# Kernel optimization log

Hardware: AMD Instinct MI355X
Metric: run time of the kernel (lower is better)

The kernel has to match this reference:

```python
import math
import jax, jax.numpy as jnp
import numpy as np

B, T, H, A, F = 2, 2048, 2048, 2048, 8192
L, LID, EPS = 24, 0, 1e-5
NEG_INF = -1e38


def setup_inputs() -> dict:
    key = jax.random.key(0)
    ks = jax.random.split(key, 8)
    s = 0.02
    # RWKV init-derived time parameters for layer_id=0, num_hidden_layers=24
    ratio_0_to_1 = LID / (L - 1)          # 0.0
    ratio_1_to_almost_0 = 1.0 - LID / L    # 1.0
    x = jnp.arange(H, dtype=jnp.float32) / H
    tmk = jnp.power(x, ratio_1_to_almost_0)
    tmv = tmk + 0.3 * ratio_0_to_1
    tmr = jnp.power(x, 0.5 * ratio_1_to_almost_0)
    zigzag = 0.5 * (jnp.arange(1, A + 1, dtype=jnp.float32) % 3 - 1)
    time_first = jnp.full((A,), math.log(0.3), dtype=jnp.float32) + zigzag
    h = jnp.arange(A, dtype=jnp.float32)
    time_decay = -5.0 + 8.0 * (h / (A - 1)) ** (0.7 + 1.3 * ratio_0_to_1)
    return {
        'hidden': jax.random.normal(ks[0], (B, T, H), jnp.float32),
        'pre_w': jnp.ones((H,), jnp.float32), 'pre_b': jnp.zeros((H,), jnp.float32),
        'ln1_w': jnp.ones((H,), jnp.float32), 'ln1_b': jnp.zeros((H,), jnp.float32),
        'ln2_w': jnp.ones((H,), jnp.float32), 'ln2_b': jnp.zeros((H,), jnp.float32),
        'time_decay': time_decay, 'time_first': time_first,
        'tmk': tmk, 'tmv': tmv, 'tmr': tmr,
        'Wk': jax.random.normal(ks[1], (H, A), jnp.float32) * s,
        'Wv': jax.random.normal(ks[2], (H, A), jnp.float32) * s,
        'Wr': jax.random.normal(ks[3], (H, A), jnp.float32) * s,
        'Wo': jax.random.normal(ks[4], (A, H), jnp.float32) * s,
        'f_tmk': jnp.power(x, ratio_1_to_almost_0), 'f_tmr': jnp.power(x, ratio_1_to_almost_0),
        'f_Wk': jax.random.normal(ks[5], (H, F), jnp.float32) * s,
        'f_Wr': jax.random.normal(ks[6], (H, H), jnp.float32) * s,
        'f_Wv': jax.random.normal(ks[7], (F, H), jnp.float32) * s,
    }


def _ln(x, w, b):
    mu = x.mean(-1, keepdims=True)
    var = ((x - mu) ** 2).mean(-1, keepdims=True)
    return (x - mu) * jax.lax.rsqrt(var + EPS) * w + b


def _token_shift(x):
    # sx state is zeros at init: prepend a zero row, drop the last token
    return jnp.concatenate((jnp.zeros_like(x[:, :1, :]), x[:, :-1, :]), axis=1)


def _forward(hidden, pre_w, pre_b, ln1_w, ln1_b, ln2_w, ln2_b,
             time_decay, time_first, tmk, tmv, tmr, Wk, Wv, Wr, Wo,
             f_tmk, f_tmr, f_Wk, f_Wr, f_Wv):
    h0 = _ln(hidden, pre_w, pre_b)          # pre_ln (layer_id == 0)
    # ---- time mixing (RwkvSelfAttention) ----
    x1 = _ln(h0, ln1_w, ln1_b)
    cx = _token_shift(x1)
    kx = x1 * tmk + cx * (1 - tmk)
    vx = x1 * tmv + cx * (1 - tmv)
    rx = x1 * tmr + cx * (1 - tmr)
    r = jax.nn.sigmoid(rx @ Wr)             # [B,T,A]
    k = kx @ Wk
    v = vx @ Wv
    w_decay = -jnp.exp(time_decay)          # [A]

    def step(carry, kv):
        aa, bb, pp = carry                  # each [B,A]
        kk, vv = kv                         # each [B,A]
        ww = time_first + kk
        q = jnp.maximum(pp, ww)
        e1 = jnp.exp(pp - q)
        e2 = jnp.exp(ww - q)
        out = (e1 * aa + e2 * vv) / (e1 * bb + e2)
        ww2 = w_decay + pp
        q2 = jnp.maximum(ww2, kk)
        e1 = jnp.exp(ww2 - q2)
        e2 = jnp.exp(kk - q2)
        return (e1 * aa + e2 * vv, e1 * bb + e2, q2), out

    init = (jnp.zeros((B, A), k.dtype), jnp.zeros((B, A), k.dtype),
            jnp.full((B, A), NEG_INF, jnp.float32))
    _, wkv = jax.lax.scan(step, init, (jnp.swapaxes(k, 0, 1), jnp.swapaxes(v, 0, 1)))
    wkv = jnp.swapaxes(wkv, 0, 1)           # [B,T,A]
    h1 = h0 + (r * wkv) @ Wo
    # ---- channel mixing (RwkvFeedForward) ----
    x2 = _ln(h1, ln2_w, ln2_b)
    cx2 = _token_shift(x2)
    kx2 = x2 * f_tmk + cx2 * (1 - f_tmk)
    rx2 = x2 * f_tmr + cx2 * (1 - f_tmr)
    r2 = jax.nn.sigmoid(rx2 @ f_Wr)
    kk2 = jnp.square(jax.nn.relu(kx2 @ f_Wk))
    return h1 + r2 * (kk2 @ f_Wv)


def reference(hidden, pre_w, pre_b, ln1_w, ln1_b, ln2_w, ln2_b,
              time_decay, time_first, tmk, tmv, tmr, Wk, Wv, Wr, Wo,
              f_tmk, f_tmr, f_Wk, f_Wr, f_Wv):
    return _forward(hidden, pre_w, pre_b, ln1_w, ln1_b, ln2_w, ln2_b,
                    time_decay, time_first, tmk, tmv, tmr, Wk, Wv, Wr, Wo,
                    f_tmk, f_tmr, f_Wk, f_Wr, f_Wv)
```

## Files before the change

kernel.cpp:

```cpp
#include <hip/hip_runtime.h>

#define B_  2
#define T_  2048
#define H_  2048
#define A_  2048
#define F_  8192
#define BT_ 4096

typedef __bf16  bf16x8 __attribute__((ext_vector_type(8)));
typedef float   f32x4  __attribute__((ext_vector_type(4)));
typedef short   short8 __attribute__((ext_vector_type(8)));

__device__ __forceinline__ float bf2f(unsigned short b) {
  return __uint_as_float(((unsigned)b) << 16);
}
__device__ __forceinline__ unsigned short f2bf(float f) {
  unsigned u = __float_as_uint(f);
  unsigned r = (u + 0x7FFFu + ((u >> 16) & 1u)) >> 16;
  return (unsigned short)r;
}

typedef __attribute__((address_space(3))) void lds_void_t;
typedef __attribute__((address_space(1))) const void gc_void_t;
__device__ __forceinline__ void gload_lds16(const void* g, void* l) {
  __builtin_amdgcn_global_load_lds((gc_void_t*)g, (lds_void_t*)l, 16, 0, 0);
}

__global__ void canary_kernel(float* out) { out[threadIdx.x] = 1000.0f; }

__global__ __launch_bounds__(256) void transpose_bf16_kernel(
    const float* __restrict__ src, unsigned short* __restrict__ dst, int Kd, int Nd)
{
  __shared__ float tile[32][33];
  const int tx = threadIdx.x & 31;
  const int ty = threadIdx.x >> 5;
  const int n0 = blockIdx.x * 32;
  const int k0 = blockIdx.y * 32;
#pragma unroll
  for (int i = 0; i < 32; i += 8)
    tile[ty + i][tx] = src[(size_t)(k0 + ty + i) * Nd + n0 + tx];
  __syncthreads();
#pragma unroll
  for (int i = 0; i < 32; i += 8)
    dst[(size_t)(n0 + ty + i) * Kd + k0 + tx] = f2bf(tile[tx][ty + i]);
}

__device__ __forceinline__ void block_reduce2(float& a, float& b) {
#pragma unroll
  for (int off = 32; off > 0; off >>= 1) {
    a += __shfl_down(a, off, 64);
    b += __shfl_down(b, off, 64);
  }
  __shared__ float sa[4], sb[4];
  const int lane = threadIdx.x & 63, w = threadIdx.x >> 6;
  __syncthreads();
  if (lane == 0) { sa[w] = a; sb[w] = b; }
  __syncthreads();
  a = sa[0] + sa[1] + sa[2] + sa[3];
  b = sb[0] + sb[1] + sb[2] + sb[3];
}

__global__ __launch_bounds__(256) void ln_pre_kernel(
    const float* __restrict__ hidden,
    const float* __restrict__ pw, const float* __restrict__ pb,
    const float* __restrict__ w1, const float* __restrict__ b1,
    float* __restrict__ h0, unsigned short* __restrict__ x1)
{
  const int row = blockIdx.x, tid = threadIdx.x;
  const int c0 = tid * 8;
  const size_t base = (size_t)row * H_ + c0;
  float x[8];
  float4 v0 = *(const float4*)(hidden + base);
  float4 v1 = *(const float4*)(hidden + base + 4);
  x[0]=v0.x; x[1]=v0.y; x[2]=v0.z; x[3]=v0.w;
  x[4]=v1.x; x[5]=v1.y; x[6]=v1.z; x[7]=v1.w;
  float s = 0.f, s2 = 0.f;
#pragma unroll
  for (int j = 0; j < 8; ++j) { s += x[j]; s2 += x[j]*x[j]; }
  block_reduce2(s, s2);
  float mu  = s * (1.f / H_);
  float inv = rsqrtf(fmaxf(s2 * (1.f / H_) - mu*mu, 0.f) + 1e-5f);
  float y[8];
#pragma unroll
  for (int j = 0; j < 8; ++j) y[j] = (x[j] - mu) * inv * pw[c0+j] + pb[c0+j];
  *(float4*)(h0 + base)     = make_float4(y[0],y[1],y[2],y[3]);
  *(float4*)(h0 + base + 4) = make_float4(y[4],y[5],y[6],y[7]);
  s = 0.f; s2 = 0.f;
#pragma unroll
  for (int j = 0; j < 8; ++j) { s += y[j]; s2 += y[j]*y[j]; }
  block_reduce2(s, s2);
  mu  = s * (1.f / H_);
  inv = rsqrtf(fmaxf(s2 * (1.f / H_) - mu*mu, 0.f) + 1e-5f);
  unsigned o[4];
#pragma unroll
  for (int p = 0; p < 4; ++p) {
    unsigned lo = f2bf((y[2*p]   - mu) * inv * w1[c0+2*p]   + b1[c0+2*p]);
    unsigned hi = f2bf((y[2*p+1] - mu) * inv * w1[c0+2*p+1] + b1[c0+2*p+1]);
    o[p] = lo | (hi << 16);
  }
  *(uint4*)(x1 + base) = make_uint4(o[0], o[1], o[2], o[3]);
}

__global__ __launch_bounds__(256) void lnmix2_kernel(
    const float* __restrict__ h1,
    const float* __restrict__ w_, const float* __restrict__ b_,
    const float* __restrict__ tmk_, const float* __restrict__ tmr_,
    unsigned short* __restrict__ kx2b, unsigned short* __restrict__ rx2b)
{
  const int row = blockIdx.x, tid = threadIdx.x;
  const int t = row & (T_ - 1);
  const int c0 = tid * 8;
  const size_t base = (size_t)row * H_ + c0;
  float x[8], p[8];
  {
    float4 v0 = *(const float4*)(h1 + base);
    float4 v1 = *(const float4*)(h1 + base + 4);
    x[0]=v0.x; x[1]=v0.y; x[2]=v0.z; x[3]=v0.w;
    x[4]=v1.x; x[5]=v1.y; x[6]=v1.z; x[7]=v1.w;
  }
  const bool hasp = (t > 0);
  if (hasp) {
    float4 v0 = *(const float4*)(h1 + base - H_);
    float4 v1 = *(const float4*)(h1 + base - H_ + 4);
    p[0]=v0.x; p[1]=v0.y; p[2]=v0.z; p[3]=v0.w;
    p[4]=v1.x; p[5]=v1.y; p[6]=v1.z; p[7]=v1.w;
  } else {
#pragma unroll
    for (int j = 0; j < 8; ++j) p[j] = 0.f;
  }
  float s = 0.f, s2 = 0.f;
#pragma unroll
  for (int j = 0; j < 8; ++j) { s += x[j]; s2 += x[j]*x[j]; }
  block_reduce2(s, s2);
  const float mu  = s * (1.f / H_);
  const float inv = rsqrtf(fmaxf(s2 * (1.f / H_) - mu*mu, 0.f) + 1e-5f);
  float sp = 0.f, sp2 = 0.f;
#pragma unroll
  for (int j = 0; j < 8; ++j) { sp += p[j]; sp2 += p[j]*p[j]; }
  block_reduce2(sp, sp2);
  const float mup  = sp * (1.f / H_);
  const float invp = rsqrtf(fmaxf(sp2 * (1.f / H_) - mup*mup, 0.f) + 1e-5f);
  unsigned ok[4], orr[4];
#pragma unroll
  for (int q = 0; q < 4; ++q) {
    unsigned ko = 0, ro = 0;
#pragma unroll
    for (int h = 0; h < 2; ++h) {
      const int j = q*2 + h;
      const float xr = (x[j] - mu) * inv * w_[c0+j] + b_[c0+j];
      const float cr = hasp ? (p[j] - mup) * invp * w_[c0+j] + b_[c0+j] : 0.f;
      ko |= (unsigned)f2bf(fmaf(xr - cr, tmk_[c0+j], cr)) << (h*16);
      ro |= (unsigned)f2bf(fmaf(xr - cr, tmr_[c0+j], cr)) << (h*16);
    }
    ok[q] = ko; orr[q] = ro;
  }
  *(uint4*)(kx2b + base) = make_uint4(ok[0],ok[1],ok[2],ok[3]);
  *(uint4*)(rx2b + base) = make_uint4(orr[0],orr[1],orr[2],orr[3]);
}

__global__ __launch_bounds__(256) void mix1_kernel(
    const unsigned short* __restrict__ x,
    const float* __restrict__ tm_,
    unsigned short* __restrict__ outb)
{
  const int row = blockIdx.x;
  const int t = row & (T_ - 1);
  const int c0 = threadIdx.x * 8;
  const size_t base = (size_t)row * H_ + c0;
  uint4 xv = *(const uint4*)(x + base);
  uint4 cv = make_uint4(0u,0u,0u,0u);
  if (t > 0) cv = *(const uint4*)(x + base - H_);
  const unsigned xs[4] = {xv.x, xv.y, xv.z, xv.w};
  const unsigned cs[4] = {cv.x, cv.y, cv.z, cv.w};
  unsigned oo[4];
#pragma unroll
  for (int p = 0; p < 4; ++p) {
    unsigned w = 0;
#pragma unroll
    for (int h = 0; h < 2; ++h) {
      const int j = p*2 + h;
      float xf = bf2f((unsigned short)((xs[p] >> (h*16)) & 0xFFFFu));
      float cf = bf2f((unsigned short)((cs[p] >> (h*16)) & 0xFFFFu));
      w |= (unsigned)f2bf(fmaf(xf - cf, tm_[c0+j], cf)) << (h*16);
    }
    oo[p] = w;
  }
  *(uint4*)(outb + base) = make_uint4(oo[0],oo[1],oo[2],oo[3]);
}

#define WKV_G 32
#define WKV_C 32
#define WKV_L 64

__global__ __launch_bounds__(1024) void wkv_scan_kernel(
    const unsigned short* __restrict__ kg, const unsigned short* __restrict__ vg,
    const unsigned short* __restrict__ rg,
    const float* __restrict__ time_first, const float* __restrict__ time_decay,
    unsigned short* __restrict__ rwkv)
{
  const int tid = threadIdx.x;
  const int al  = tid & (WKV_G - 1);
  const int c   = tid >> 5;
  const int b   = blockIdx.x >> 6;
  const int ag  = blockIdx.x & 63;
  const int a   = ag * WKV_G + al;
  const float tf = time_first[a];
  const float w  = -__expf(time_decay[a]);
  const size_t cb = (size_t)b * T_ * A_ + a + (size_t)c * WKV_L * A_;

  float aa = 0.f, bb = 0.f, pp = -1e38f;
  {
    float kb[4], vb[4];
#pragma unroll
    for (int j = 0; j < 4; ++j) {
      kb[j] = bf2f(kg[cb + (size_t)j * A_]);
      vb[j] = bf2f(vg[cb + (size_t)j * A_]);
    }
    for (int t0 = 0; t0 < WKV_L; t0 += 4) {
#pragma unroll
      for (int j = 0; j < 4; ++j) {
        const float kk = kb[j], vv = vb[j];
        const int tn = t0 + j + 4;
        if (tn < WKV_L) {
          kb[j] = bf2f(kg[cb + (size_t)tn * A_]);
          vb[j] = bf2f(vg[cb + (size_t)tn * A_]);
        }
        float ww2 = w + pp;
        float q2  = fmaxf(ww2, kk);
        float e1  = __expf(ww2 - q2);
        float e2  = __expf(kk  - q2);
        aa = e1*aa + e2*vv;
        bb = e1*bb + e2;
        pp = q2;
      }
    }
  }
  __shared__ float saa[WKV_C][WKV_G], sbb[WKV_C][WKV_G], spp[WKV_C][WKV_G];
  saa[c][al] = aa; sbb[c][al] = bb; spp[c][al] = pp;
  __syncthreads();

  if (tid < WKV_G) {
    float Aa = 0.f, Bb = 0.f, Pp = -1e38f;
    const float Lw = (float)WKV_L * w;
    for (int cc = 0; cc < WKV_C; ++cc) {
      const float na = saa[cc][tid], nb = sbb[cc][tid], np = spp[cc][tid];
      saa[cc][tid] = Aa; sbb[cc][tid] = Bb; spp[cc][tid] = Pp;
      const float p1 = Pp + Lw;
      const float pc = fmaxf(p1, np);
      const float f1 = __expf(p1 - pc);
      const float f2 = __expf(np - pc);
      Aa = f1*Aa + f2*na;
      Bb = f1*Bb + f2*nb;
      Pp = pc;
    }
  }
  __syncthreads();
  aa = saa[c][al]; bb = sbb[c][al]; pp = spp[c][al];

  {
    float kb[4], vb[4], rb[4];
#pragma unroll
    for (int j = 0; j < 4; ++j) {
      kb[j] = bf2f(kg[cb + (size_t)j * A_]);
      vb[j] = bf2f(vg[cb + (size_t)j * A_]);
      rb[j] = bf2f(rg[cb + (size_t)j * A_]);
    }
    for (int t0 = 0; t0 < WKV_L; t0 += 4) {
#pragma unroll
      for (int j = 0; j < 4; ++j) {
        const float kk = kb[j], vv = vb[j], rr = rb[j];
        const int tn = t0 + j + 4;
        if (tn < WKV_L) {
          kb[j] = bf2f(kg[cb + (size_t)tn * A_]);
          vb[j] = bf2f(vg[cb + (size_t)tn * A_]);
          rb[j] = bf2f(rg[cb + (size_t)tn * A_]);
        }
        float ww = tf + kk;
        float q  = fmaxf(pp, ww);
        float e1 = __expf(pp - q);
        float e2 = __expf(ww - q);
        float o  = (e1*aa + e2*vv) / (e1*bb + e2);
        float sr = 1.f / (1.f + __expf(-rr));
        rwkv[cb + (size_t)(t0 + j) * A_] = f2bf(sr * o);
        float ww2 = w + pp;
        float q2  = fmaxf(ww2, kk);
        e1 = __expf(ww2 - q2);
        e2 = __expf(kk  - q2);
        aa = e1*aa + e2*vv;
        bb = e1*bb + e2;
        pp = q2;
      }
    }
  }
}

enum { EPI_BF16 = 0, EPI_ADDIP = 1, EPI_RELU2 = 2, EPI_SIGADD = 3 };

template <int BM, int NBUF, int RG, int CG, int EPI>
__global__ __launch_bounds__(512) void gemm4_kernel(
    const unsigned short* __restrict__ Ap, const unsigned short* __restrict__ Bp,
    void* __restrict__ Cp, int K, int Nn,
    const unsigned short* __restrict__ sigb)
{
  constexpr int BN = 256;
  constexpr int FM = BM / 32;
  constexpr int FN = 4;
  __shared__ unsigned short As[NBUF * BM * 64];
  __shared__ unsigned short Bs[NBUF * BN * 64];
  const int tid  = threadIdx.x;
  const int lane = tid & 63;
  const int lr = lane & 15;
  const int hi = lane >> 4;
  const int rx7 = lr & 7;
  const int wid = tid >> 6;
  const int wm = wid >> 2, wn = wid & 3;
  const int rowW = wm * (BM / 2);
  const int colW = wn * 64;
  const int gx = gridDim.x;
  const int gy = gridDim.y;
  const int flat = blockIdx.y * gx + blockIdx.x;
  const int xcd = flat & 7;
  const int j = flat >> 3;
  const int rgc = gy / RG;
  const int r_idx = xcd % rgc;
  const int c_idx = xcd / rgc;
  const int row_l = j % RG;
  const int col_l = j / RG;
  const long row0 = (long)(r_idx * RG + row_l) * BM;
  const long col0 = (long)(c_idx * CG + col_l) * BN;
  const unsigned short* Ab = Ap + (size_t)row0 * K;
  const unsigned short* Bb = Bp + (size_t)col0 * K;
  const int srow8 = tid >> 3;
  const int sslot = (tid & 7) ^ (srow8 & 7);
  f32x4 acc[FM][FN] = {};

  auto SP0 = [&](int bufi, int tt) {
    unsigned short* asb = As + bufi * (BM * 64);
    unsigned short* bsb = Bs + bufi * (BN * 64);
    const size_t ko = (size_t)tt * 64 + sslot * 8;
    gload_lds16(Ab + (size_t)srow8        * K + ko, asb + tid * 8);
    gload_lds16(Ab + (size_t)(srow8 + 64) * K + ko, asb + 4096 + tid * 8);
    gload_lds16(Bb + (size_t)srow8        * K + ko, bsb + tid * 8);
  };
  auto SP1 = [&](int bufi, int tt) {
    unsigned short* bsb = Bs + bufi * (BN * 64);
    const size_t ko = (size_t)tt * 64 + sslot * 8;
    gload_lds16(Bb + (size_t)(srow8 + 64)  * K + ko, bsb + 4096  + tid * 8);
    gload_lds16(Bb + (size_t)(srow8 + 128) * K + ko, bsb + 8192  + tid * 8);
    gload_lds16(Bb + (size_t)(srow8 + 192) * K + ko, bsb + 12288 + tid * 8);
  };
  auto SPq = [&](int bufi, int tt, int q) {
    const size_t ko = (size_t)tt * 64 + sslot * 8;
    if (q < 2) {
      unsigned short* asb = As + bufi * (BM * 64);
      gload_lds16(Ab + (size_t)(srow8 + q*128)      * K + ko, asb + q*8192 + tid * 8);
      gload_lds16(Ab + (size_t)(srow8 + q*128 + 64) * K + ko, asb + q*8192 + 4096 + tid * 8);
    } else {
      const int qq = q - 2;
      unsigned short* bsb = Bs + bufi * (BN * 64);
      gload_lds16(Bb + (size_t)(srow8 + qq*128)      * K + ko, bsb + qq*8192 + tid * 8);
      gload_lds16(Bb + (size_t)(srow8 + qq*128 + 64) * K + ko, bsb + qq*8192 + 4096 + tid * 8);
    }
  };

  const int nt = K >> 6;
  if constexpr (BM == 128) {
    SP0(0, 0); SP1(0, 0);
    if constexpr (NBUF == 3) { SP0(1, 1); SP1(1, 1); }
  } else {
#pragma unroll
    for (int q = 0; q < 4; ++q) SPq(0, 0, q);
  }
  int cur = 0;
  for (int t = 0; t < nt; ++t) {
    if constexpr (NBUF == 3) {
      if (t + 1 < nt) asm volatile("s_waitcnt vmcnt(6)" ::: "memory");
      else            asm volatile("s_waitcnt vmcnt(0)" ::: "memory");
    } else {
      asm volatile("s_waitcnt vmcnt(0)" ::: "memory");
    }
    __builtin_amdgcn_s_barrier();
    int nb = cur + (NBUF - 1); if (nb >= NBUF) nb -= NBUF;
    const unsigned short* asb = As + cur * (BM * 64);
    const unsigned short* bsb = Bs + cur * (BN * 64);
    if constexpr (BM == 128) {
      bf16x8 af0[4], bf0[4], af1[4], bf1[4];
      const int p0 = (0*4 + hi) ^ rx7;
      const int p1 = (1*4 + hi) ^ rx7;
#pragma unroll
      for (int m = 0; m < 4; ++m)
        af0[m] = __builtin_bit_cast(bf16x8,
            *(const short8*)(asb + (rowW + m*16 + lr) * 64 + p0*8));
#pragma unroll
      for (int n = 0; n < 4; ++n)
        bf0[n] = __builtin_bit_cast(bf16x8,
            *(const short8*)(bsb + (colW + n*16 + lr) * 64 + p0*8));
#pragma unroll
      for (int m = 0; m < 4; ++m)
        af1[m] = __builtin_bit_cast(bf16x8,
            *(const short8*)(asb + (rowW + m*16 + lr) * 64 + p1*8));
#pragma unroll
      for (int n = 0; n < 4; ++n)
        bf1[n] = __builtin_bit_cast(bf16x8,
            *(const short8*)(bsb + (colW + n*16 + lr) * 64 + p1*8));
      if (t + NBUF - 1 < nt) SP0(nb, t + NBUF - 1);
      asm volatile("s_waitcnt lgkmcnt(8)" ::: "memory");
      __builtin_amdgcn_sched_barrier(0);
      __builtin_amdgcn_s_setprio(1);
#pragma unroll
      for (int m = 0; m < 4; ++m)
#pragma unroll
        for (int n = 0; n < 4; ++n)
          acc[m][n] = __builtin_amdgcn_mfma_f32_16x16x32_bf16(af0[m], bf0[n], acc[m][n], 0, 0, 0);
      __builtin_amdgcn_s_setprio(0);
      if (t + NBUF - 1 < nt) SP1(nb, t + NBUF - 1);
      asm volatile("s_waitcnt lgkmcnt(0)" ::: "memory");
      __builtin_amdgcn_sched_barrier(0);
      __builtin_amdgcn_s_setprio(1);
#pragma unroll
      for (int m = 0; m < 4; ++m)
#pragma unroll
        for (int n = 0; n < 4; ++n)
          acc[m][n] = __builtin_amdgcn_mfma_f32_16x16x32_bf16(af1[m], bf1[n], acc[m][n], 0, 0, 0);
      __builtin_amdgcn_s_setprio(0);
    } else {
      bf16x8 bfrk[4];
#pragma unroll
      for (int sub = 0; sub < 4; ++sub) {
        const int kk = sub >> 1, mh = sub & 1;
        bf16x8 af[4];
#pragma unroll
        for (int m = 0; m < 4; ++m) {
          const int row = rowW + (mh*4 + m)*16 + lr;
          const int ps = (kk*4 + hi) ^ rx7;
          af[m] = __builtin_bit_cast(bf16x8, *(const short8*)(asb + row*64 + ps*8));
        }
        if (mh == 0) {
#pragma unroll
          for (int n = 0; n < 4; ++n) {
            const int row = colW + n*16 + lr;
            const int ps = (kk*4 + hi) ^ rx7;
            bfrk[n] = __builtin_bit_cast(bf16x8, *(const short8*)(bsb + row*64 + ps*8));
          }
        }
        if (t + 1 < nt) SPq(nb, t + 1, sub);
        asm volatile("s_waitcnt lgkmcnt(0)" ::: "memory");
        __builtin_amdgcn_sched_barrier(0);
        __builtin_amdgcn_s_setprio(1);
#pragma unroll
        for (int m = 0; m < 4; ++m)
#pragma unroll
          for (int n = 0; n < 4; ++n)
            acc[mh*4 + m][n] = __builtin_amdgcn_mfma_f32_16x16x32_bf16(af[m], bfrk[n], acc[mh*4 + m][n], 0, 0, 0);
        __builtin_amdgcn_s_setprio(0);
      }
    }
    cur = (cur + 1 == NBUF) ? 0 : cur + 1;
  }

#pragma unroll
  for (int m = 0; m < FM; ++m) {
#pragma unroll
    for (int n = 0; n < FN; ++n) {
      const long col = col0 + colW + n*16 + lr;
#pragma unroll
      for (int j2 = 0; j2 < 4; ++j2) {
        const long row = row0 + rowW + m*16 + hi*4 + j2;
        const size_t idx = (size_t)row * Nn + col;
        const float v = acc[m][n][j2];
        if (EPI == EPI_BF16) {
          ((unsigned short*)Cp)[idx] = f2bf(v);
        } else if (EPI == EPI_ADDIP) {
          float* C = (float*)Cp;
          C[idx] = C[idx] + v;
        } else if (EPI == EPI_RELU2) {
          float rr = v > 0.f ? v : 0.f;
          ((unsigned short*)Cp)[idx] = f2bf(rr * rr);
        } else {
          float s = 1.f / (1.f + __expf(-bf2f(sigb[idx])));
          float* C = (float*)Cp;
          C[idx] = C[idx] + s * v;
        }
      }
    }
  }
}

#define MB(x) ((size_t)(x) << 20)
#define WS_NEED MB(184)

extern "C" void kernel_launch(void* const* d_in, const int* in_sizes, int n_in,
                              void* d_out, int out_size, void* d_ws, size_t ws_size,
                              hipStream_t stream) {
  const float* hidden     = (const float*)d_in[0];
  const float* pre_w      = (const float*)d_in[1];
  const float* pre_b      = (const float*)d_in[2];
  const float* ln1_w      = (const float*)d_in[3];
  const float* ln1_b      = (const float*)d_in[4];
  const float* ln2_w      = (const float*)d_in[5];
  const float* ln2_b      = (const float*)d_in[6];
  const float* time_decay = (const float*)d_in[7];
  const float* time_first = (const float*)d_in[8];
  const float* tmk        = (const float*)d_in[9];
  const float* tmv        = (const float*)d_in[10];
  const float* tmr        = (const float*)d_in[11];
  const float* Wk         = (const float*)d_in[12];
  const float* Wv         = (const float*)d_in[13];
  const float* Wr         = (const float*)d_in[14];
  const float* Wo         = (const float*)d_in[15];
  const float* f_tmk      = (const float*)d_in[16];
  const float* f_tmr      = (const float*)d_in[17];
  const float* f_Wk       = (const float*)d_in[18];
  const float* f_Wr       = (const float*)d_in[19];
  const float* f_Wv       = (const float*)d_in[20];
  float* out = (float*)d_out;
  char*  ws  = (char*)d_ws;

  if (ws_size < WS_NEED) {
    canary_kernel<<<1, 256, 0, stream>>>(out);
    return;
  }

  unsigned short* fWkT = (unsigned short*)(ws + MB(0));
  unsigned short* fWvT = (unsigned short*)(ws + MB(32));
  unsigned short* WkT  = (unsigned short*)(ws + MB(64));
  unsigned short* WvT  = (unsigned short*)(ws + MB(72));
  unsigned short* WrT  = (unsigned short*)(ws + MB(80));
  unsigned short* WoT  = (unsigned short*)(ws + MB(88));
  unsigned short* fWrT = (unsigned short*)(ws + MB(96));
  unsigned short* KK   = (unsigned short*)(ws + MB(64));
  unsigned short* S1   = (unsigned short*)(ws + MB(104));
  unsigned short* S4   = (unsigned short*)(ws + MB(120));
  unsigned short* S2   = (unsigned short*)(ws + MB(136));
  unsigned short* S3   = (unsigned short*)(ws + MB(152));
  unsigned short* M1   = (unsigned short*)(ws + MB(168));

  const dim3 blk(256);
  const dim3 blk512(512);
  const dim3 gSmall(8, 32);
  const dim3 gRelu(32, 16);

  transpose_bf16_kernel<<<dim3(64, 64),  blk, 0, stream>>>(Wk,   WkT,  2048, 2048);
  transpose_bf16_kernel<<<dim3(64, 64),  blk, 0, stream>>>(Wv,   WvT,  2048, 2048);
  transpose_bf16_kernel<<<dim3(64, 64),  blk, 0, stream>>>(Wr,   WrT,  2048, 2048);
  transpose_bf16_kernel<<<dim3(64, 64),  blk, 0, stream>>>(Wo,   WoT,  2048, 2048);
  transpose_bf16_kernel<<<dim3(64, 64),  blk, 0, stream>>>(f_Wr, fWrT, 2048, 2048);
  transpose_bf16_kernel<<<dim3(256, 64), blk, 0, stream>>>(f_Wk, fWkT, 2048, 8192);
  transpose_bf16_kernel<<<dim3(64, 256), blk, 0, stream>>>(f_Wv, fWvT, 8192, 2048);

  ln_pre_kernel<<<BT_, blk, 0, stream>>>(hidden, pre_w, pre_b, ln1_w, ln1_b, out, S1);

  mix1_kernel<<<BT_, blk, 0, stream>>>(S1, tmk, M1);
  gemm4_kernel<128,3,8,4,EPI_BF16><<<gSmall, blk512, 0, stream>>>(M1, WkT, S2, 2048, 2048, nullptr);
  mix1_kernel<<<BT_, blk, 0, stream>>>(S1, tmv, M1);
  gemm4_kernel<128,3,8,4,EPI_BF16><<<gSmall, blk512, 0, stream>>>(M1, WvT, S3, 2048, 2048, nullptr);
  mix1_kernel<<<BT_, blk, 0, stream>>>(S1, tmr, M1);
  gemm4_kernel<128,3,8,4,EPI_BF16><<<gSmall, blk512, 0, stream>>>(M1, WrT, S4, 2048, 2048, nullptr);

  wkv_scan_kernel<<<dim3(128), dim3(1024), 0, stream>>>(S2, S3, S4, time_first, time_decay, S1);

  gemm4_kernel<128,3,8,4,EPI_ADDIP><<<gSmall, blk512, 0, stream>>>(S1, WoT, out, 2048, 2048, nullptr);

  lnmix2_kernel<<<BT_, blk, 0, stream>>>(out, ln2_w, ln2_b, f_tmk, f_tmr, M1, S2);

  gemm4_kernel<128,3,8,4,EPI_BF16><<<gSmall, blk512, 0, stream>>>(S2, fWrT, S3, 2048, 2048, nullptr);

  gemm4_kernel<256,2,8,8,EPI_RELU2><<<gRelu, blk512, 0, stream>>>(M1, fWkT, KK, 2048, 8192, nullptr);

  gemm4_kernel<128,3,8,4,EPI_SIGADD><<<gSmall, blk512, 0, stream>>>(KK, fWvT, out, 8192, 2048, S3);
}
```

Measured before the change: 656.5 us.

## Fuse three token-shift mixes and batch K/V/R GEMMs via grid z

Replaces three separate mix kernels with one that reads the normalized input once and writes the k, v and r mixes. The three projection GEMMs become a single launch using blockIdx.z with per-slice byte offsets for A, B and C, so more blocks run at once and launch overhead drops. The BM=256 GEMM inner loop is rewritten to double-buffer LDS fragment reads with partial lgkmcnt waits, so MFMAs overlap the next loads. Workspace buffers are reordered so the large FFN weight transposes run after the batched GEMM, which adds some risk of aliasing mistakes.

```diff
diff --git a/kernel.cpp b/kernel.cpp
--- a/kernel.cpp
+++ b/kernel.cpp
@@ -158,10 +158,10 @@
   *(uint4*)(rx2b + base) = make_uint4(orr[0],orr[1],orr[2],orr[3]);
 }
 
-__global__ __launch_bounds__(256) void mix1_kernel(
+__global__ __launch_bounds__(256) void mix3_kernel(
     const unsigned short* __restrict__ x,
-    const float* __restrict__ tm_,
-    unsigned short* __restrict__ outb)
+    const float* __restrict__ mk_, const float* __restrict__ mv_, const float* __restrict__ mr_,
+    unsigned short* __restrict__ kx, unsigned short* __restrict__ vx, unsigned short* __restrict__ rx)
 {
   const int row = blockIdx.x;
   const int t = row & (T_ - 1);
@@ -172,20 +172,25 @@
   if (t > 0) cv = *(const uint4*)(x + base - H_);
   const unsigned xs[4] = {xv.x, xv.y, xv.z, xv.w};
   const unsigned cs[4] = {cv.x, cv.y, cv.z, cv.w};
-  unsigned oo[4];
+  unsigned ok[4], ov[4], orr[4];
 #pragma unroll
   for (int p = 0; p < 4; ++p) {
-    unsigned w = 0;
+    unsigned ko=0, vo=0, ro=0;
 #pragma unroll
     for (int h = 0; h < 2; ++h) {
       const int j = p*2 + h;
       float xf = bf2f((unsigned short)((xs[p] >> (h*16)) & 0xFFFFu));
       float cf = bf2f((unsigned short)((cs[p] >> (h*16)) & 0xFFFFu));
-      w |= (unsigned)f2bf(fmaf(xf - cf, tm_[c0+j], cf)) << (h*16);
-    }
-    oo[p] = w;
-  }
-  *(uint4*)(outb + base) = make_uint4(oo[0],oo[1],oo[2],oo[3]);
+      float d  = xf - cf;
+      ko |= (unsigned)f2bf(fmaf(d, mk_[c0+j], cf)) << (h*16);
+      vo |= (unsigned)f2bf(fmaf(d, mv_[c0+j], cf)) << (h*16);
+      ro |= (unsigned)f2bf(fmaf(d, mr_[c0+j], cf)) << (h*16);
+    }
+    ok[p]=ko; ov[p]=vo; orr[p]=ro;
+  }
+  *(uint4*)(kx + base) = make_uint4(ok[0],ok[1],ok[2],ok[3]);
+  *(uint4*)(vx + base) = make_uint4(ov[0],ov[1],ov[2],ov[3]);
+  *(uint4*)(rx + base) = make_uint4(orr[0],orr[1],orr[2],orr[3]);
 }
 
 #define WKV_G 32
@@ -300,13 +305,18 @@
 __global__ __launch_bounds__(512) void gemm4_kernel(
     const unsigned short* __restrict__ Ap, const unsigned short* __restrict__ Bp,
     void* __restrict__ Cp, int K, int Nn,
-    const unsigned short* __restrict__ sigb)
+    const unsigned short* __restrict__ sigb,
+    size_t azB, size_t bzB, size_t czB)
 {
   constexpr int BN = 256;
   constexpr int FM = BM / 32;
   constexpr int FN = 4;
   __shared__ unsigned short As[NBUF * BM * 64];
   __shared__ unsigned short Bs[NBUF * BN * 64];
+  const int zz = blockIdx.z;
+  Ap = (const unsigned short*)((const char*)Ap + zz * azB);
+  Bp = (const unsigned short*)((const char*)Bp + zz * bzB);
+  Cp = (void*)((char*)Cp + zz * czB);
   const int tid  = threadIdx.x;
   const int lane = tid & 63;
   const int lr = lane & 15;
@@ -424,36 +434,73 @@
           acc[m][n] = __builtin_amdgcn_mfma_f32_16x16x32_bf16(af1[m], bf1[n], acc[m][n], 0, 0, 0);
       __builtin_amdgcn_s_setprio(0);
     } else {
-      bf16x8 bfrk[4];
-#pragma unroll
-      for (int sub = 0; sub < 4; ++sub) {
-        const int kk = sub >> 1, mh = sub & 1;
-        bf16x8 af[4];
-#pragma unroll
-        for (int m = 0; m < 4; ++m) {
-          const int row = rowW + (mh*4 + m)*16 + lr;
-          const int ps = (kk*4 + hi) ^ rx7;
-          af[m] = __builtin_bit_cast(bf16x8, *(const short8*)(asb + row*64 + ps*8));
-        }
-        if (mh == 0) {
-#pragma unroll
-          for (int n = 0; n < 4; ++n) {
-            const int row = colW + n*16 + lr;
-            const int ps = (kk*4 + hi) ^ rx7;
-            bfrk[n] = __builtin_bit_cast(bf16x8, *(const short8*)(bsb + row*64 + ps*8));
-          }
-        }
-        if (t + 1 < nt) SPq(nb, t + 1, sub);
-        asm volatile("s_waitcnt lgkmcnt(0)" ::: "memory");
-        __builtin_amdgcn_sched_barrier(0);
-        __builtin_amdgcn_s_setprio(1);
-#pragma unroll
-        for (int m = 0; m < 4; ++m)
-#pragma unroll
-          for (int n = 0; n < 4; ++n)
-            acc[mh*4 + m][n] = __builtin_amdgcn_mfma_f32_16x16x32_bf16(af[m], bfrk[n], acc[mh*4 + m][n], 0, 0, 0);
-        __builtin_amdgcn_s_setprio(0);
-      }
+      bf16x8 aF[2][4], bF[2][4];
+      const int p0 = (0*4 + hi) ^ rx7;
+      const int p1 = (1*4 + hi) ^ rx7;
+#pragma unroll
+      for (int n = 0; n < 4; ++n)
+        bF[0][n] = __builtin_bit_cast(bf16x8,
+            *(const short8*)(bsb + (colW + n*16 + lr) * 64 + p0*8));
+#pragma unroll
+      for (int m = 0; m < 4; ++m)
+        aF[0][m] = __builtin_bit_cast(bf16x8,
+            *(const short8*)(asb + (rowW + m*16 + lr) * 64 + p0*8));
+#pragma unroll
+      for (int m = 0; m < 4; ++m)
+        aF[1][m] = __builtin_bit_cast(bf16x8,
+            *(const short8*)(asb + (rowW + (4+m)*16 + lr) * 64 + p0*8));
+      if (t + 1 < nt) SPq(nb, t + 1, 0);
+      asm volatile("s_waitcnt lgkmcnt(4)" ::: "memory");
+      __builtin_amdgcn_sched_barrier(0);
+      __builtin_amdgcn_s_setprio(1);
+#pragma unroll
+      for (int m = 0; m < 4; ++m)
+#pragma unroll
+        for (int n = 0; n < 4; ++n)
+          acc[m][n] = __builtin_amdgcn_mfma_f32_16x16x32_bf16(aF[0][m], bF[0][n], acc[m][n], 0, 0, 0);
+      __builtin_amdgcn_s_setprio(0);
+#pragma unroll
+      for (int n = 0; n < 4; ++n)
+        bF[1][n] = __builtin_bit_cast(bf16x8,
+            *(const short8*)(bsb + (colW + n*16 + lr) * 64 + p1*8));
+#pragma unroll
+      for (int m = 0; m < 4; ++m)
+        aF[0][m] = __builtin_bit_cast(bf16x8,
+            *(const short8*)(asb + (rowW + m*16 + lr) * 64 + p1*8));
+      if (t + 1 < nt) SPq(nb, t + 1, 1);
+      asm volatile("s_waitcnt lgkmcnt(8)" ::: "memory");
+      __builtin_amdgcn_sched_barrier(0);
+      __builtin_amdgcn_s_setprio(1);
+#pragma unroll
+      for (int m = 0; m < 4; ++m)
+#pragma unroll
+        for (int n = 0; n < 4; ++n)
+          acc[4+m][n] = __builtin_amdgcn_mfma_f32_16x16x32_bf16(aF[1][m], bF[0][n], acc[4+m][n], 0, 0, 0);
+      __builtin_amdgcn_s_setprio(0);
+#pragma unroll
+      for (int m = 0; m < 4; ++m)
+        aF[1][m] = __builtin_bit_cast(bf16x8,
+            *(const short8*)(asb + (rowW + (4+m)*16 + lr) * 64 + p1*8));
+      if (t + 1 < nt) SPq(nb, t + 1, 2);
+      asm volatile("s_waitcnt lgkmcnt(4)" ::: "memory");
+      __builtin_amdgcn_sched_barrier(0);
+      __builtin_amdgcn_s_setprio(1);
+#pragma unroll
+      for (int m = 0; m < 4; ++m)
+#pragma unroll
+        for (int n = 0; n < 4; ++n)
+          acc[m][n] = __builtin_amdgcn_mfma_f32_16x16x32_bf16(aF[0][m], bF[1][n], acc[m][n], 0, 0, 0);
+      __builtin_amdgcn_s_setprio(0);
+      if (t + 1 < nt) SPq(nb, t + 1, 3);
+      asm volatile("s_waitcnt lgkmcnt(0)" ::: "memory");
+      __builtin_amdgcn_sched_barrier(0);
+      __builtin_amdgcn_s_setprio(1);
+#pragma unroll
+      for (int m = 0; m < 4; ++m)
+#pragma unroll
+        for (int n = 0; n < 4; ++n)
+          acc[4+m][n] = __builtin_amdgcn_mfma_f32_16x16x32_bf16(aF[1][m], bF[1][n], acc[4+m][n], 0, 0, 0);
+      __builtin_amdgcn_s_setprio(0);
     }
     cur = (cur + 1 == NBUF) ? 0 : cur + 1;
   }
@@ -521,51 +568,53 @@
     return;
   }
 
+  unsigned short* MX   = (unsigned short*)(ws + MB(0));
   unsigned short* fWkT = (unsigned short*)(ws + MB(0));
   unsigned short* fWvT = (unsigned short*)(ws + MB(32));
   unsigned short* WkT  = (unsigned short*)(ws + MB(64));
-  unsigned short* WvT  = (unsigned short*)(ws + MB(72));
-  unsigned short* WrT  = (unsigned short*)(ws + MB(80));
   unsigned short* WoT  = (unsigned short*)(ws + MB(88));
   unsigned short* fWrT = (unsigned short*)(ws + MB(96));
   unsigned short* KK   = (unsigned short*)(ws + MB(64));
   unsigned short* S1   = (unsigned short*)(ws + MB(104));
-  unsigned short* S4   = (unsigned short*)(ws + MB(120));
-  unsigned short* S2   = (unsigned short*)(ws + MB(136));
-  unsigned short* S3   = (unsigned short*)(ws + MB(152));
+  unsigned short* kbuf = (unsigned short*)(ws + MB(120));
+  unsigned short* vbuf = (unsigned short*)(ws + MB(136));
+  unsigned short* rbuf = (unsigned short*)(ws + MB(152));
   unsigned short* M1   = (unsigned short*)(ws + MB(168));
 
   const dim3 blk(256);
   const dim3 blk512(512);
   const dim3 gSmall(8, 32);
+  const dim3 gSmall3(8, 32, 3);
   const dim3 gRelu(32, 16);
 
-  transpose_bf16_kernel<<<dim3(64, 64),  blk, 0, stream>>>(Wk,   WkT,  2048, 2048);
-  transpose_bf16_kernel<<<dim3(64, 64),  blk, 0, stream>>>(Wv,   WvT,  2048, 2048);
-  transpose_bf16_kernel<<<dim3(64, 64),  blk, 0, stream>>>(Wr,   WrT,  2048, 2048);
-  transpose_bf16_kernel<<<dim3(64, 64),  blk, 0, stream>>>(Wo,   WoT,  2048, 2048);
-  transpose_bf16_kernel<<<dim3(64, 64),  blk, 0, stream>>>(f_Wr, fWrT, 2048, 2048);
+  transpose_bf16_kernel<<<dim3(64, 64),  blk, 0, stream>>>(Wk,   WkT,                              2048, 2048);
+  transpose_bf16_kernel<<<dim3(64, 64),  blk, 0, stream>>>(Wv,   (unsigned short*)(ws + MB(72)),  2048, 2048);
+  transpose_bf16_kernel<<<dim3(64, 64),  blk, 0, stream>>>(Wr,   (unsigned short*)(ws + MB(80)),  2048, 2048);
+  transpose_bf16_kernel<<<dim3(64, 64),  blk, 0, stream>>>(Wo,   WoT,                              2048, 2048);
+  transpose_bf16_kernel<<<dim3(64, 64),  blk, 0, stream>>>(f_Wr, fWrT,                             2048, 2048);
+
+  ln_pre_kernel<<<BT_, blk, 0, stream>>>(hidden, pre_w, pre_b, ln1_w, ln1_b, out, S1);
+
+  mix3_kernel<<<BT_, blk, 0, stream>>>(S1, tmk, tmv, tmr, MX, MX + (MB(16)>>1), MX + (MB(32)>>1));
+  gemm4_kernel<128,3,8,4,EPI_BF16><<<gSmall3, blk512, 0, stream>>>(
+      MX, WkT, kbuf, 2048, 2048, nullptr, MB(16), MB(8), MB(16));
+
   transpose_bf16_kernel<<<dim3(256, 64), blk, 0, stream>>>(f_Wk, fWkT, 2048, 8192);
   transpose_bf16_kernel<<<dim3(64, 256), blk, 0, stream>>>(f_Wv, fWvT, 8192, 2048);
 
-  ln_pre_kernel<<<BT_, blk, 0, stream>>>(hidden, pre_w, pre_b, ln1_w, ln1_b, out, S1);
-
-  mix1_kernel<<<BT_, blk, 0, stream>>>(S1, tmk, M1);
-  gemm4_kernel<128,3,8,4,EPI_BF16><<<gSmall, blk512, 0, stream>>>(M1, WkT, S2, 2048, 2048, nullptr);
-  mix1_kernel<<<BT_, blk, 0, stream>>>(S1, tmv, M1);
-  gemm4_kernel<128,3,8,4,EPI_BF16><<<gSmall, blk512, 0, stream>>>(M1, WvT, S3, 2048, 2048, nullptr);
-  mix1_kernel<<<BT_, blk, 0, stream>>>(S1, tmr, M1);
-  gemm4_kernel<128,3,8,4,EPI_BF16><<<gSmall, blk512, 0, stream>>>(M1, WrT, S4, 2048, 2048, nullptr);
-
-  wkv_scan_kernel<<<dim3(128), dim3(1024), 0, stream>>>(S2, S3, S4, time_first, time_decay, S1);
-
-  gemm4_kernel<128,3,8,4,EPI_ADDIP><<<gSmall, blk512, 0, stream>>>(S1, WoT, out, 2048, 2048, nullptr);
-
-  lnmix2_kernel<<<BT_, blk, 0, stream>>>(out, ln2_w, ln2_b, f_tmk, f_tmr, M1, S2);
-
-  gemm4_kernel<128,3,8,4,EPI_BF16><<<gSmall, blk512, 0, stream>>>(S2, fWrT, S3, 2048, 2048, nullptr);
-
-  gemm4_kernel<256,2,8,8,EPI_RELU2><<<gRelu, blk512, 0, stream>>>(M1, fWkT, KK, 2048, 8192, nullptr);
-
-  gemm4_kernel<128,3,8,4,EPI_SIGADD><<<gSmall, blk512, 0, stream>>>(KK, fWvT, out, 8192, 2048, S3);
-}
+  wkv_scan_kernel<<<dim3(128), dim3(1024), 0, stream>>>(kbuf, vbuf, rbuf, time_first, time_decay, S1);
+
+  gemm4_kernel<128,3,8,4,EPI_ADDIP><<<gSmall, blk512, 0, stream>>>(
+      S1, WoT, out, 2048, 2048, nullptr, 0, 0, 0);
+
+  lnmix2_kernel<<<BT_, blk, 0, stream>>>(out, ln2_w, ln2_b, f_tmk, f_tmr, M1, kbuf);
+
+  gemm4_kernel<128,3,8,4,EPI_BF16><<<gSmall, blk512, 0, stream>>>(
+      kbuf, fWrT, vbuf, 2048, 2048, nullptr, 0, 0, 0);
+
+  gemm4_kernel<256,2,8,8,EPI_RELU2><<<gRelu, blk512, 0, stream>>>(
+      M1, fWkT, KK, 2048, 8192, nullptr, 0, 0, 0);
+
+  gemm4_kernel<128,3,8,4,EPI_SIGADD><<<gSmall, blk512, 0, stream>>>(
+      KK, fWvT, out, 8192, 2048, vbuf, 0, 0, 0);
+}
```

New measurement: 642.4 us. -2.2%, faster.
